# Kernel tuning notes

Hardware: AMD Instinct MI355X
Metric: run time of the kernel (lower is better)

Reference implementation:

```python
import jax, jax.numpy as jnp
import numpy as np
from jax import lax

# Straight-through sign: forward sign(x), backward passes grad where |x|<=1 (hardtanh STE)
@jax.custom_vjp
def sign_ste(x):
    return jnp.sign(x)

def _sign_fwd(x):
    return jnp.sign(x), x

def _sign_bwd(x, g):
    return (g * (jnp.abs(x) <= 1.0).astype(g.dtype),)

sign_ste.defvjp(_sign_fwd, _sign_bwd)

STRIDE = 1
PADDING = 1

def setup_inputs() -> dict:
    key = jax.random.key(0)
    k1, k2, k3 = jax.random.split(key, 3)
    B, Cin, H, W = 32, 256, 56, 56
    Cout, K = 256, 3
    inp = jax.random.normal(k1, (B, Cin, H, W), dtype=jnp.float32)
    # kaiming-uniform-ish init like torch Conv2d default
    fan_in = Cin * K * K
    bound = 1.0 / np.sqrt(fan_in)
    weight1 = jax.random.uniform(k2, (Cout, Cin, K, K), minval=-bound, maxval=bound, dtype=jnp.float32)
    weight2 = jax.random.uniform(k3, (Cout, Cin, K, K), minval=-bound, maxval=bound, dtype=jnp.float32)
    return {"input": inp, "weight1": weight1, "weight2": weight2}

def reference(input, weight1, weight2):
    # ternarized weight: (sign(w1)+sign(w2))/2 in {-1,-0.5,0,0.5,1}
    w_ter = (sign_ste(weight1) + sign_ste(weight2)) * 0.5
    x_bin = sign_ste(input)
    out = lax.conv_general_dilated(
        x_bin, w_ter,
        window_strides=(STRIDE, STRIDE),
        padding=[(PADDING, PADDING), (PADDING, PADDING)],
        dimension_numbers=("NCHW", "OIHW", "NCHW"),
    )
    # per-output-channel scaling: mean|w1| + mean|w2| over (in, kh, kw)
    alpha = jnp.mean(jnp.abs(weight1), axis=(1, 2, 3)) + jnp.mean(jnp.abs(weight2), axis=(1, 2, 3))
    return out * alpha[None, :, None, None]
```

## Files before the change

kernel.cpp:

```cpp
#include <hip/hip_runtime.h>
#include <hip/hip_bf16.h>

#define B_    32
#define C_    256
#define H_    56
#define W_    56
#define HP    58
#define WPAD  58
#define HW    3136
#define CHW   802816
#define M_TOT 100352

typedef __bf16 bf16;
typedef __bf16 bf16x8 __attribute__((ext_vector_type(8)));
typedef float floatx4 __attribute__((ext_vector_type(4)));

#define XPAD_ELEMS (B_ * HP * WPAD * C_)
#define XPAD_BYTES (XPAD_ELEMS * 2)
#define WPK_ELEMS  (C_ * 9 * C_)
#define WPK_BYTES  (WPK_ELEMS * 2)

__global__ __launch_bounds__(256) void pack_w_kernel(const float* __restrict__ w1,
                                                     const float* __restrict__ w2,
                                                     bf16* __restrict__ wp,
                                                     float* __restrict__ alpha) {
  const int co = blockIdx.x;
  const int ci = threadIdx.x;
  const int base = (co * C_ + ci) * 9;
  float sabs = 0.f;
#pragma unroll
  for (int s = 0; s < 9; ++s) {
    const float a = w1[base + s];
    const float b = w2[base + s];
    const float sa = (a > 0.f) ? 1.f : ((a < 0.f) ? -1.f : 0.f);
    const float sb = (b > 0.f) ? 1.f : ((b < 0.f) ? -1.f : 0.f);
    wp[(co * 9 + s) * C_ + ci] = (bf16)(0.5f * (sa + sb));
    sabs += fabsf(a) + fabsf(b);
  }
#pragma unroll
  for (int off = 32; off > 0; off >>= 1) sabs += __shfl_down(sabs, off, 64);
  __shared__ float red[4];
  if ((threadIdx.x & 63) == 0) red[threadIdx.x >> 6] = sabs;
  __syncthreads();
  if (threadIdx.x == 0)
    alpha[co] = (red[0] + red[1] + red[2] + red[3]) * (1.0f / 2304.0f);
}

#define ROWP 264
__global__ __launch_bounds__(256) void pack_x_kernel(const float* __restrict__ in,
                                                     bf16* __restrict__ xp) {
  __shared__ bf16 row[58 * ROWP];
  const int yp = blockIdx.x % HP;
  const int b  = blockIdx.x / HP;
  const int tid = threadIdx.x;

  float4* rz = (float4*)row;
  const float4 z4 = make_float4(0.f, 0.f, 0.f, 0.f);
#pragma unroll
  for (int i = 0; i < 8; ++i) {
    const int idx = i * 256 + tid;
    if (idx < (58 * ROWP * 2) / 16) rz[idx] = z4;
  }
  __syncthreads();

  const int y = yp - 1;
  if (y >= 0 && y < H_) {
    const int x = tid & 63;
    const int cig = tid >> 6;
    if (x < W_) {
#pragma unroll
      for (int it = 0; it < 8; ++it) {
        const int ci0 = it * 32 + cig * 8;
        bf16x8 v;
#pragma unroll
        for (int j = 0; j < 8; ++j) {
          const float f = in[((b * C_ + ci0 + j) * H_ + y) * W_ + x];
          v[j] = (bf16)((f > 0.f) ? 1.f : ((f < 0.f) ? -1.f : 0.f));
        }
        *(bf16x8*)&row[(x + 1) * ROWP + ci0] = v;
      }
    }
  }
  __syncthreads();

  const int cc = tid & 31;
  const int xo = tid >> 5;
  bf16* dst = xp + (size_t)(b * HP + yp) * WPAD * C_;
#pragma unroll
  for (int it = 0; it < 8; ++it) {
    const int xs = it * 8 + xo;
    if (xs < WPAD)
      *(float4*)(dst + xs * C_ + cc * 8) = *(const float4*)&row[xs * ROWP + cc * 8];
  }
}

__global__ __launch_bounds__(256, 2) void gemm_kernel(const bf16* __restrict__ xp,
                                                      const bf16* __restrict__ wp,
                                                      const float* __restrict__ alpha,
                                                      float* __restrict__ out) {
  __shared__ bf16 sA[128 * 64];
  __shared__ bf16 sB[128 * 64];
  const int tid = threadIdx.x;

  const int id = blockIdx.x;
  const int xcd = id & 7;
  const int l = id >> 3;
  const int co0 = (l & 1) * 128;
  const int m0 = ((l >> 1) * 8 + xcd) * 128;

  const int srow = tid >> 3;
  const int scol = (tid & 7) ^ (srow & 7);

  const bf16* wsrc[4];
  const bf16* xsrc[4];
#pragma unroll
  for (int i = 0; i < 4; ++i) {
    const int m = m0 + srow + 32 * i;
    const int b = m / HW;
    const int rem = m - b * HW;
    const int y = rem / W_;
    const int x = rem - y * W_;
    xsrc[i] = xp + ((b * HP + y) * WPAD + x) * C_ + scol * 8;
    wsrc[i] = wp + (co0 + srow + 32 * i) * 9 * C_ + scol * 8;
  }

  floatx4 acc[4][4] = {};

  const int lane = tid & 63;
  const int wave = tid >> 6;
  const int wm = wave >> 1;
  const int wn = wave & 1;
  const int lrow = lane & 15;
  const int quad = lane >> 4;
  const int swk = lrow & 7;
  const char* sAc = (const char*)sA;
  const char* sBc = (const char*)sB;
  const int abase = (wm * 64 + lrow) * 128;
  const int bbase = (wn * 64 + lrow) * 128;

  for (int s = 0; s < 9; ++s) {
    const int shoff = ((s / 3) * WPAD + (s % 3)) * C_;
    for (int kc = 0; kc < 4; ++kc) {
      const int ci0 = kc * 64;
      __syncthreads();
#pragma unroll
      for (int i = 0; i < 4; ++i) {
        __builtin_amdgcn_global_load_lds(
            (const __attribute__((address_space(1))) void*)(wsrc[i] + s * C_ + ci0),
            (__attribute__((address_space(3))) void*)((char*)sA + i * 4096 + tid * 16),
            16, 0, 0);
      }
#pragma unroll
      for (int i = 0; i < 4; ++i) {
        __builtin_amdgcn_global_load_lds(
            (const __attribute__((address_space(1))) void*)(xsrc[i] + shoff + ci0),
            (__attribute__((address_space(3))) void*)((char*)sB + i * 4096 + tid * 16),
            16, 0, 0);
      }
      __syncthreads();
#pragma unroll
      for (int kf = 0; kf < 2; ++kf) {
        const int coff = (((kf << 2) + quad) ^ swk) << 4;
        bf16x8 af[4], bfv[4];
#pragma unroll
        for (int i = 0; i < 4; ++i)
          af[i] = *(const bf16x8*)(sAc + abase + i * 2048 + coff);
#pragma unroll
        for (int j = 0; j < 4; ++j)
          bfv[j] = *(const bf16x8*)(sBc + bbase + j * 2048 + coff);
#pragma unroll
        for (int i = 0; i < 4; ++i)
#pragma unroll
          for (int j = 0; j < 4; ++j)
            acc[i][j] = __builtin_amdgcn_mfma_f32_16x16x32_bf16(af[i], bfv[j],
                                                                acc[i][j], 0, 0, 0);
      }
    }
  }

  int ob[4];
#pragma unroll
  for (int j = 0; j < 4; ++j) {
    const int m = m0 + wn * 64 + j * 16 + lrow;
    const int b = m / HW;
    const int rem = m - b * HW;
    const int y = rem / W_;
    const int x = rem - y * W_;
    ob[j] = b * CHW + y * W_ + x;
  }
#pragma unroll
  for (int i = 0; i < 4; ++i) {
#pragma unroll
    for (int r = 0; r < 4; ++r) {
      const int co = co0 + wm * 64 + i * 16 + quad * 4 + r;
      const float sc = alpha[co];
#pragma unroll
      for (int j = 0; j < 4; ++j)
        out[ob[j] + co * HW] = acc[i][j][r] * sc;
    }
  }
}

extern "C" void kernel_launch(void* const* d_in, const int* in_sizes, int n_in,
                              void* d_out, int out_size, void* d_ws, size_t ws_size,
                              hipStream_t stream) {
  const float* input = (const float*)d_in[0];
  const float* w1 = (const float*)d_in[1];
  const float* w2 = (const float*)d_in[2];
  float* out = (float*)d_out;

  char* ws = (char*)d_ws;
  bf16* xp = (bf16*)ws;
  bf16* wp = (bf16*)(ws + XPAD_BYTES);
  float* alpha = (float*)(ws + XPAD_BYTES + WPK_BYTES);

  pack_w_kernel<<<C_, 256, 0, stream>>>(w1, w2, wp, alpha);
  pack_x_kernel<<<B_ * HP, 256, 0, stream>>>(input, xp);
  gemm_kernel<<<M_TOT / 128 * (C_ / 128), 256, 0, stream>>>(xp, wp, alpha, out);
}
```

Measured before the change: 291.5 us.

## Switch binarized conv GEMM from bf16 to int8 MFMA

Packs the sign-binarized activations and the ternary weights (stored as sign(w1)+sign(w2), with the 0.5 folded into alpha) as int8 instead of bf16. The GEMM uses the i32 16x16x64 int8 MFMA, which does twice the K per instruction and moves half the bytes per tile, so each filter tap needs 2 K-chunks instead of 4. Results stay exact because the values are small integers. Launch bounds are raised to 3 blocks per CU, and the pack kernels are retuned for 16-byte char vectors.

```diff
diff --git a/kernel.cpp b/kernel.cpp
--- a/kernel.cpp
+++ b/kernel.cpp
@@ -11,19 +11,16 @@
 #define CHW   802816
 #define M_TOT 100352
 
-typedef __bf16 bf16;
-typedef __bf16 bf16x8 __attribute__((ext_vector_type(8)));
-typedef float floatx4 __attribute__((ext_vector_type(4)));
-
-#define XPAD_ELEMS (B_ * HP * WPAD * C_)
-#define XPAD_BYTES (XPAD_ELEMS * 2)
-#define WPK_ELEMS  (C_ * 9 * C_)
-#define WPK_BYTES  (WPK_ELEMS * 2)
+typedef char charx16 __attribute__((ext_vector_type(16)));
+typedef int  intx4   __attribute__((ext_vector_type(4)));
+
+#define XPAD_BYTES (B_ * HP * WPAD * C_)
+#define WPK_BYTES  (C_ * 9 * C_)
 
 __global__ __launch_bounds__(256) void pack_w_kernel(const float* __restrict__ w1,
                                                      const float* __restrict__ w2,
-                                                     bf16* __restrict__ wp,
-                                                     float* __restrict__ alpha) {
+                                                     char* __restrict__ wq,
+                                                     float* __restrict__ alphah) {
   const int co = blockIdx.x;
   const int ci = threadIdx.x;
   const int base = (co * C_ + ci) * 9;
@@ -32,9 +29,9 @@
   for (int s = 0; s < 9; ++s) {
     const float a = w1[base + s];
     const float b = w2[base + s];
-    const float sa = (a > 0.f) ? 1.f : ((a < 0.f) ? -1.f : 0.f);
-    const float sb = (b > 0.f) ? 1.f : ((b < 0.f) ? -1.f : 0.f);
-    wp[(co * 9 + s) * C_ + ci] = (bf16)(0.5f * (sa + sb));
+    const int sa = (a > 0.f) - (a < 0.f);
+    const int sb = (b > 0.f) - (b < 0.f);
+    wq[(co * 9 + s) * C_ + ci] = (char)(sa + sb);
     sabs += fabsf(a) + fabsf(b);
   }
 #pragma unroll
@@ -43,13 +40,13 @@
   if ((threadIdx.x & 63) == 0) red[threadIdx.x >> 6] = sabs;
   __syncthreads();
   if (threadIdx.x == 0)
-    alpha[co] = (red[0] + red[1] + red[2] + red[3]) * (1.0f / 2304.0f);
-}
-
-#define ROWP 264
+    alphah[co] = (red[0] + red[1] + red[2] + red[3]) * (0.5f / 2304.0f);
+}
+
+#define ROWPC 272
 __global__ __launch_bounds__(256) void pack_x_kernel(const float* __restrict__ in,
-                                                     bf16* __restrict__ xp) {
-  __shared__ bf16 row[58 * ROWP];
+                                                     char* __restrict__ xp) {
+  __shared__ char row[58 * ROWPC];
   const int yp = blockIdx.x % HP;
   const int b  = blockIdx.x / HP;
   const int tid = threadIdx.x;
@@ -57,49 +54,48 @@
   float4* rz = (float4*)row;
   const float4 z4 = make_float4(0.f, 0.f, 0.f, 0.f);
 #pragma unroll
-  for (int i = 0; i < 8; ++i) {
+  for (int i = 0; i < 4; ++i) {
     const int idx = i * 256 + tid;
-    if (idx < (58 * ROWP * 2) / 16) rz[idx] = z4;
+    if (idx < (58 * ROWPC) / 16) rz[idx] = z4;
   }
   __syncthreads();
 
   const int y = yp - 1;
-  if (y >= 0 && y < H_) {
-    const int x = tid & 63;
-    const int cig = tid >> 6;
-    if (x < W_) {
-#pragma unroll
-      for (int it = 0; it < 8; ++it) {
-        const int ci0 = it * 32 + cig * 8;
-        bf16x8 v;
-#pragma unroll
-        for (int j = 0; j < 8; ++j) {
-          const float f = in[((b * C_ + ci0 + j) * H_ + y) * W_ + x];
-          v[j] = (bf16)((f > 0.f) ? 1.f : ((f < 0.f) ? -1.f : 0.f));
-        }
-        *(bf16x8*)&row[(x + 1) * ROWP + ci0] = v;
-      }
+  const int x = tid & 63;
+  const int cig = tid >> 6;
+  if (y >= 0 && y < H_ && x < W_) {
+    const float* src = in + ((size_t)(b * C_) * H_ + y) * W_ + x;
+#pragma unroll
+    for (int it = 0; it < 4; ++it) {
+      const int ci0 = it * 64 + cig * 16;
+      charx16 v;
+#pragma unroll
+      for (int j = 0; j < 16; ++j) {
+        const float f = src[(size_t)(ci0 + j) * HW];
+        v[j] = (char)((f > 0.f) - (f < 0.f));
+      }
+      *(charx16*)&row[(x + 1) * ROWPC + ci0] = v;
     }
   }
   __syncthreads();
 
-  const int cc = tid & 31;
-  const int xo = tid >> 5;
-  bf16* dst = xp + (size_t)(b * HP + yp) * WPAD * C_;
-#pragma unroll
-  for (int it = 0; it < 8; ++it) {
-    const int xs = it * 8 + xo;
+  const int cc = tid & 15;
+  const int xo = tid >> 4;
+  char* dst = xp + (size_t)(b * HP + yp) * WPAD * C_;
+#pragma unroll
+  for (int it = 0; it < 4; ++it) {
+    const int xs = it * 16 + xo;
     if (xs < WPAD)
-      *(float4*)(dst + xs * C_ + cc * 8) = *(const float4*)&row[xs * ROWP + cc * 8];
-  }
-}
-
-__global__ __launch_bounds__(256, 2) void gemm_kernel(const bf16* __restrict__ xp,
-                                                      const bf16* __restrict__ wp,
-                                                      const float* __restrict__ alpha,
+      *(float4*)(dst + xs * C_ + cc * 16) = *(const float4*)&row[xs * ROWPC + cc * 16];
+  }
+}
+
+__global__ __launch_bounds__(256, 3) void gemm_kernel(const char* __restrict__ xp,
+                                                      const char* __restrict__ wq,
+                                                      const float* __restrict__ alphah,
                                                       float* __restrict__ out) {
-  __shared__ bf16 sA[128 * 64];
-  __shared__ bf16 sB[128 * 64];
+  __shared__ char sA[128 * 128];
+  __shared__ char sB[128 * 128];
   const int tid = threadIdx.x;
 
   const int id = blockIdx.x;
@@ -111,8 +107,8 @@
   const int srow = tid >> 3;
   const int scol = (tid & 7) ^ (srow & 7);
 
-  const bf16* wsrc[4];
-  const bf16* xsrc[4];
+  const char* wsrc[4];
+  const char* xsrc[4];
 #pragma unroll
   for (int i = 0; i < 4; ++i) {
     const int m = m0 + srow + 32 * i;
@@ -120,11 +116,11 @@
     const int rem = m - b * HW;
     const int y = rem / W_;
     const int x = rem - y * W_;
-    xsrc[i] = xp + ((b * HP + y) * WPAD + x) * C_ + scol * 8;
-    wsrc[i] = wp + (co0 + srow + 32 * i) * 9 * C_ + scol * 8;
-  }
-
-  floatx4 acc[4][4] = {};
+    xsrc[i] = xp + ((b * HP + y) * WPAD + x) * C_ + scol * 16;
+    wsrc[i] = wq + (co0 + srow + 32 * i) * 9 * C_ + scol * 16;
+  }
+
+  intx4 acc[4][4] = {};
 
   const int lane = tid & 63;
   const int wave = tid >> 6;
@@ -133,47 +129,47 @@
   const int lrow = lane & 15;
   const int quad = lane >> 4;
   const int swk = lrow & 7;
-  const char* sAc = (const char*)sA;
-  const char* sBc = (const char*)sB;
   const int abase = (wm * 64 + lrow) * 128;
   const int bbase = (wn * 64 + lrow) * 128;
 
   for (int s = 0; s < 9; ++s) {
+    const int woff = s * C_;
     const int shoff = ((s / 3) * WPAD + (s % 3)) * C_;
-    for (int kc = 0; kc < 4; ++kc) {
-      const int ci0 = kc * 64;
+#pragma unroll
+    for (int h = 0; h < 2; ++h) {
+      const int hh = h * 128;
       __syncthreads();
 #pragma unroll
       for (int i = 0; i < 4; ++i) {
         __builtin_amdgcn_global_load_lds(
-            (const __attribute__((address_space(1))) void*)(wsrc[i] + s * C_ + ci0),
-            (__attribute__((address_space(3))) void*)((char*)sA + i * 4096 + tid * 16),
+            (const __attribute__((address_space(1))) void*)(wsrc[i] + woff + hh),
+            (__attribute__((address_space(3))) void*)(sA + i * 4096 + tid * 16),
             16, 0, 0);
       }
 #pragma unroll
       for (int i = 0; i < 4; ++i) {
         __builtin_amdgcn_global_load_lds(
-            (const __attribute__((address_space(1))) void*)(xsrc[i] + shoff + ci0),
-            (__attribute__((address_space(3))) void*)((char*)sB + i * 4096 + tid * 16),
+            (const __attribute__((address_space(1))) void*)(xsrc[i] + shoff + hh),
+            (__attribute__((address_space(3))) void*)(sB + i * 4096 + tid * 16),
             16, 0, 0);
       }
       __syncthreads();
 #pragma unroll
       for (int kf = 0; kf < 2; ++kf) {
         const int coff = (((kf << 2) + quad) ^ swk) << 4;
-        bf16x8 af[4], bfv[4];
+        intx4 af[4], bfv[4];
 #pragma unroll
         for (int i = 0; i < 4; ++i)
-          af[i] = *(const bf16x8*)(sAc + abase + i * 2048 + coff);
+          af[i] = *(const intx4*)(sA + abase + i * 2048 + coff);
 #pragma unroll
         for (int j = 0; j < 4; ++j)
-          bfv[j] = *(const bf16x8*)(sBc + bbase + j * 2048 + coff);
+          bfv[j] = *(const intx4*)(sB + bbase + j * 2048 + coff);
 #pragma unroll
         for (int i = 0; i < 4; ++i)
 #pragma unroll
           for (int j = 0; j < 4; ++j)
-            acc[i][j] = __builtin_amdgcn_mfma_f32_16x16x32_bf16(af[i], bfv[j],
-                                                                acc[i][j], 0, 0, 0);
+            acc[i][j] = __builtin_amdgcn_mfma_i32_16x16x64_i8(af[i], bfv[j],
+                                                              acc[i][j], 0, 0, 0);
       }
     }
   }
@@ -193,10 +189,10 @@
 #pragma unroll
     for (int r = 0; r < 4; ++r) {
       const int co = co0 + wm * 64 + i * 16 + quad * 4 + r;
-      const float sc = alpha[co];
+      const float sc = alphah[co];
 #pragma unroll
       for (int j = 0; j < 4; ++j)
-        out[ob[j] + co * HW] = acc[i][j][r] * sc;
+        out[ob[j] + co * HW] = (float)acc[i][j][r] * sc;
     }
   }
 }
@@ -210,11 +206,11 @@
   float* out = (float*)d_out;
 
   char* ws = (char*)d_ws;
-  bf16* xp = (bf16*)ws;
-  bf16* wp = (bf16*)(ws + XPAD_BYTES);
-  float* alpha = (float*)(ws + XPAD_BYTES + WPK_BYTES);
-
-  pack_w_kernel<<<C_, 256, 0, stream>>>(w1, w2, wp, alpha);
+  char* xp = ws;
+  char* wq = ws + XPAD_BYTES;
+  float* alphah = (float*)(ws + XPAD_BYTES + WPK_BYTES);
+
+  pack_w_kernel<<<C_, 256, 0, stream>>>(w1, w2, wq, alphah);
   pack_x_kernel<<<B_ * HP, 256, 0, stream>>>(input, xp);
-  gemm_kernel<<<M_TOT / 128 * (C_ / 128), 256, 0, stream>>>(xp, wp, alpha, out);
-}
+  gemm_kernel<<<M_TOT / 128 * (C_ / 128), 256, 0, stream>>>(xp, wq, alphah, out);
+}
```

After: 251.6 us. 1.16x faster.
